# Performance work log

Measured on AMD Instinct MI355X. Metric: run time of the kernel, lower is better.

Reference implementation:

```python
import jax, jax.numpy as jnp
import numpy as np

B, N, C_IN, C_OUT, R_IN, R_OUT, NUM_PSI, E = 4, 1024, 128, 256, 32, 32, 2, 65536


def psi(x, src, dst, W, b):
    # GIN-style GNN layer: aggregate neighbors via scatter-add, then linear+relu
    agg = jax.ops.segment_sum(x[src], dst, num_segments=x.shape[0])
    return jax.nn.relu((x + agg) @ W + b)


def setup_inputs() -> dict:
    key = jax.random.key(0)
    ks = jax.random.split(key, 12)
    inp = {
        'x_s': jax.random.normal(ks[0], (B * N, C_IN), jnp.float32),
        'edge_index_s': jax.random.randint(ks[1], (2, E), 0, B * N, jnp.int32),
        'x_t': jax.random.normal(ks[2], (B * N, C_IN), jnp.float32),
        'edge_index_t': jax.random.randint(ks[3], (2, E), 0, B * N, jnp.int32),
        'r': jax.random.normal(ks[4], (NUM_PSI, B, N, R_IN), jnp.float32),
        'W1': jax.random.normal(ks[5], (C_IN, C_OUT), jnp.float32) * (0.2 / np.sqrt(C_IN)),
        'b1': jnp.zeros((C_OUT,), jnp.float32),
        'Wp': jax.random.normal(ks[6], (NUM_PSI, R_IN, R_OUT), jnp.float32) * (1.0 / np.sqrt(R_IN)),
        'bp': jnp.zeros((NUM_PSI, R_OUT), jnp.float32),
        'Wm1': jax.random.normal(ks[7], (R_OUT, R_OUT), jnp.float32) * (1.0 / np.sqrt(R_OUT)),
        'bm1': jnp.zeros((R_OUT,), jnp.float32),
        'Wm2': jax.random.normal(ks[8], (R_OUT, 1), jnp.float32) * (1.0 / np.sqrt(R_OUT)),
        'bm2': jnp.zeros((1,), jnp.float32),
        'sum_weights': jnp.ones((NUM_PSI + 1,), jnp.float32),
    }
    return inp


def reference(x_s, edge_index_s, x_t, edge_index_t, r, W1, b1, Wp, bp, Wm1, bm1, Wm2, bm2, sum_weights):
    src_s, dst_s = edge_index_s[0], edge_index_s[1]
    src_t, dst_t = edge_index_t[0], edge_index_t[1]
    # psi_1 node embeddings, then dense-batch (equal-size graphs -> masks all true)
    h_s = psi(x_s, src_s, dst_s, W1, b1).reshape(B, N, C_OUT)
    h_t = psi(x_t, src_t, dst_t, W1, b1).reshape(B, N, C_OUT)
    S_hat = jnp.einsum('bsc,btc->bst', h_s, h_t)  # [B, N_s, N_t]
    S_0 = jax.nn.softmax(S_hat, axis=-1)
    S_stack = []
    for i in range(NUM_PSI):  # structurally distinct psi modules
        S = jax.nn.softmax(S_hat, axis=-1)
        r_s = r[i]  # [B, N, R_IN] random node indicators
        r_t = jnp.einsum('bst,bsr->btr', S, r_s)
        o_s = psi(r_s.reshape(B * N, R_IN), src_s, dst_s, Wp[i], bp[i]).reshape(B, N, R_OUT)
        o_t = psi(r_t.reshape(B * N, R_IN), src_t, dst_t, Wp[i], bp[i]).reshape(B, N, R_OUT)
        D = o_s[:, :, None, :] - o_t[:, None, :, :]  # [B, N_s, N_t, R_OUT]
        upd = (jax.nn.relu(D @ Wm1 + bm1) @ Wm2 + bm2)[..., 0]
        S_hat = S_hat + upd
        S_stack.append(jax.nn.softmax(S_hat, axis=-1))
    S_final = sum_weights[0] * S_0
    for i in range(NUM_PSI):
        S_final = S_final + sum_weights[i + 1] * S_stack[i]
    return jax.nn.softmax(S_final.reshape(B * N, N), axis=-1)
```

## Files before the change

kernel.cpp:

```cpp
#include <hip/hip_runtime.h>
#include <hip/hip_bf16.h>

#define NBATCH 4
#define NSEQ   1024
#define BNN    4096
#define CIN    128
#define COUT   256
#define RDIM   32
#define NEDGE  65536

__global__ void edge_hist(const int* __restrict__ ei_s, const int* __restrict__ ei_t,
                          int* __restrict__ cnt) {
    int gid = blockIdx.x * blockDim.x + threadIdx.x;
    int list = gid >> 16;
    int e = gid & (NEDGE - 1);
    const int* ei = list ? ei_t : ei_s;
    atomicAdd(&cnt[list * BNN + ei[NEDGE + e]], 1);
}

__global__ void edge_scan(const int* __restrict__ cnt, int* __restrict__ offs,
                          int* __restrict__ cursor) {
    __shared__ int sums[256];
    int list = blockIdx.x;
    int tid = threadIdx.x;
    int local[16];
    int s = 0;
#pragma unroll
    for (int k = 0; k < 16; k++) { local[k] = cnt[list * BNN + tid * 16 + k]; s += local[k]; }
    sums[tid] = s;
    __syncthreads();
    for (int off = 1; off < 256; off <<= 1) {
        int v = 0;
        if (tid >= off) v = sums[tid - off];
        __syncthreads();
        if (tid >= off) sums[tid] += v;
        __syncthreads();
    }
    int run = tid ? sums[tid - 1] : 0;
#pragma unroll
    for (int k = 0; k < 16; k++) {
        offs[list * (BNN + 1) + tid * 16 + k] = run;
        cursor[list * BNN + tid * 16 + k] = run;
        run += local[k];
    }
    if (tid == 255) offs[list * (BNN + 1) + BNN] = run;
}

__global__ void edge_place(const int* __restrict__ ei_s, const int* __restrict__ ei_t,
                           int* __restrict__ cursor, int* __restrict__ ssrc) {
    int gid = blockIdx.x * blockDim.x + threadIdx.x;
    int list = gid >> 16;
    int e = gid & (NEDGE - 1);
    const int* ei = list ? ei_t : ei_s;
    int dst = ei[NEDGE + e], src = ei[e];
    int p = atomicAdd(&cursor[list * BNN + dst], 1);
    ssrc[list * NEDGE + p] = src;
}

__global__ void gather_agg128(const float* __restrict__ x_s, const float* __restrict__ x_t,
                              const int* __restrict__ offs, const int* __restrict__ ssrc,
                              float* __restrict__ t_s, float* __restrict__ t_t) {
    __shared__ int sl[128];
    int node = blockIdx.x & (BNN - 1);
    int list = blockIdx.x >> 12;
    const float* x = list ? x_t : x_s;
    float* t = list ? t_t : t_s;
    int c = threadIdx.x;
    int beg = offs[list * (BNN + 1) + node], end = offs[list * (BNN + 1) + node + 1];
    float acc = x[(size_t)node * CIN + c];
    for (int base = beg; base < end; base += 128) {
        int cnt = min(128, end - base);
        __syncthreads();
        if (c < cnt) sl[c] = ssrc[list * NEDGE + base + c];
        __syncthreads();
        int e = 0;
        for (; e + 4 <= cnt; e += 4) {
            int n0 = sl[e], n1 = sl[e + 1], n2 = sl[e + 2], n3 = sl[e + 3];
            acc += x[(size_t)n0 * CIN + c] + x[(size_t)n1 * CIN + c]
                 + x[(size_t)n2 * CIN + c] + x[(size_t)n3 * CIN + c];
        }
        for (; e < cnt; e++) acc += x[(size_t)sl[e] * CIN + c];
    }
    t[(size_t)node * CIN + c] = acc;
}

__global__ void gather_agg32(const float* __restrict__ rs, const float* __restrict__ rtin,
                             const int* __restrict__ offs, const int* __restrict__ ssrc,
                             float* __restrict__ trs, float* __restrict__ trt) {
    int list = blockIdx.y;
    int node = blockIdx.x * 8 + (threadIdx.x >> 5);
    int c = threadIdx.x & 31;
    const float* in = list ? rtin : rs;
    float* outp = list ? trt : trs;
    int beg = offs[list * (BNN + 1) + node], end = offs[list * (BNN + 1) + node + 1];
    float acc = in[(size_t)node * RDIM + c];
    for (int e = beg; e < end; e++)
        acc += in[(size_t)ssrc[list * NEDGE + e] * RDIM + c];
    outp[(size_t)node * RDIM + c] = acc;
}

__global__ void psi1_gemm(const float* __restrict__ t_s, const float* __restrict__ t_t,
                          const float* __restrict__ W1, const float* __restrict__ b1,
                          float* __restrict__ h_s, float* __restrict__ h_t) {
    __shared__ float rows[8][CIN];
    int half = blockIdx.x >> 9;
    const float* t = half ? t_t : t_s;
    float* h = half ? h_t : h_s;
    int r0 = (blockIdx.x & 511) * 8;
    int tid = threadIdx.x;
    {
        int rr = tid >> 5, c4 = (tid & 31) << 2;
        *(float4*)&rows[rr][c4] = *(const float4*)(t + (size_t)(r0 + rr) * CIN + c4);
    }
    __syncthreads();
    float acc[8];
    float bias = b1[tid];
#pragma unroll
    for (int r = 0; r < 8; r++) acc[r] = bias;
    for (int k = 0; k < CIN; k++) {
        float w = W1[k * COUT + tid];
#pragma unroll
        for (int r = 0; r < 8; r++) acc[r] = fmaf(rows[r][k], w, acc[r]);
    }
#pragma unroll
    for (int r = 0; r < 8; r++)
        h[(size_t)(r0 + r) * COUT + tid] = fmaxf(acc[r], 0.f);
}

__global__ __launch_bounds__(256) void shat_gemm(const float* __restrict__ hs,
                                                 const float* __restrict__ ht,
                                                 float* __restrict__ Sh) {
    __shared__ float As[16][132];
    __shared__ float Bs[16][68];
    int b  = blockIdx.z;
    int s0 = blockIdx.y * 128, t0 = blockIdx.x * 64;
    const float* A  = hs + (size_t)b * NSEQ * COUT;
    const float* Bm = ht + (size_t)b * NSEQ * COUT;
    int tid = threadIdx.x;
    int tx = tid & 15, ty = tid >> 4;
    int lrA = tid >> 1,  lkA = (tid & 1) * 8;
    int lrB = tid >> 2,  lkB = (tid & 3) * 4;
    const float* Ap = A  + (size_t)(s0 + lrA) * COUT + lkA;
    const float* Bp = Bm + (size_t)(t0 + lrB) * COUT + lkB;
    float4 a0 = *(const float4*)(Ap);
    float4 a1 = *(const float4*)(Ap + 4);
    float4 b0 = *(const float4*)(Bp);
    float acc[8][4] = {};
    for (int kp = 0; kp < 16; kp++) {
        __syncthreads();
        As[lkA + 0][lrA] = a0.x; As[lkA + 1][lrA] = a0.y;
        As[lkA + 2][lrA] = a0.z; As[lkA + 3][lrA] = a0.w;
        As[lkA + 4][lrA] = a1.x; As[lkA + 5][lrA] = a1.y;
        As[lkA + 6][lrA] = a1.z; As[lkA + 7][lrA] = a1.w;
        Bs[lkB + 0][lrB] = b0.x; Bs[lkB + 1][lrB] = b0.y;
        Bs[lkB + 2][lrB] = b0.z; Bs[lkB + 3][lrB] = b0.w;
        __syncthreads();
        if (kp < 15) {
            a0 = *(const float4*)(Ap + (kp + 1) * 16);
            a1 = *(const float4*)(Ap + (kp + 1) * 16 + 4);
            b0 = *(const float4*)(Bp + (kp + 1) * 16);
        }
#pragma unroll
        for (int k = 0; k < 16; k++) {
            float av[8], bv[4];
            *(float4*)&av[0] = *(const float4*)&As[k][ty * 8];
            *(float4*)&av[4] = *(const float4*)&As[k][ty * 8 + 4];
            *(float4*)&bv[0] = *(const float4*)&Bs[k][tx * 4];
#pragma unroll
            for (int i = 0; i < 8; i++)
#pragma unroll
                for (int j = 0; j < 4; j++)
                    acc[i][j] = fmaf(av[i], bv[j], acc[i][j]);
        }
    }
#pragma unroll
    for (int i = 0; i < 8; i++) {
        float4 v = make_float4(acc[i][0], acc[i][1], acc[i][2], acc[i][3]);
        *(float4*)(Sh + ((size_t)b * NSEQ + s0 + ty * 8 + i) * NSEQ + t0 + tx * 4) = v;
    }
}

__global__ void softmax_stats(const float* __restrict__ Sh, float* __restrict__ mstat,
                              float* __restrict__ istat) {
    int row = blockIdx.x, tid = threadIdx.x;
    float4 v = *(const float4*)(Sh + (size_t)row * NSEQ + tid * 4);
    float m = fmaxf(fmaxf(v.x, v.y), fmaxf(v.z, v.w));
#pragma unroll
    for (int o = 32; o; o >>= 1) m = fmaxf(m, __shfl_xor(m, o));
    __shared__ float redm[4], reds[4];
    int wid = tid >> 6, lane = tid & 63;
    if (lane == 0) redm[wid] = m;
    __syncthreads();
    m = fmaxf(fmaxf(redm[0], redm[1]), fmaxf(redm[2], redm[3]));
    float s = __expf(v.x - m) + __expf(v.y - m) + __expf(v.z - m) + __expf(v.w - m);
#pragma unroll
    for (int o = 32; o; o >>= 1) s += __shfl_xor(s, o);
    if (lane == 0) reds[wid] = s;
    __syncthreads();
    if (tid == 0) {
        float tot = reds[0] + reds[1] + reds[2] + reds[3];
        mstat[row] = m;
        istat[row] = 1.0f / tot;
    }
}

__global__ void softmax_final3(const float* __restrict__ Sh0, const float* __restrict__ Sh1,
                               const float* __restrict__ Sh2, const float* __restrict__ m0a,
                               const float* __restrict__ i0a, const float* __restrict__ m1a,
                               const float* __restrict__ i1a, const float* __restrict__ sw,
                               float* __restrict__ out) {
    int row = blockIdx.x, tid = threadIdx.x;
    __shared__ float red[4];
    int wid = tid >> 6, lane = tid & 63;
    float4 v0 = *(const float4*)(Sh0 + (size_t)row * NSEQ + tid * 4);
    float4 v1 = *(const float4*)(Sh1 + (size_t)row * NSEQ + tid * 4);
    float4 v2 = *(const float4*)(Sh2 + (size_t)row * NSEQ + tid * 4);
    float m2 = fmaxf(fmaxf(v2.x, v2.y), fmaxf(v2.z, v2.w));
#pragma unroll
    for (int o = 32; o; o >>= 1) m2 = fmaxf(m2, __shfl_xor(m2, o));
    if (lane == 0) red[wid] = m2;
    __syncthreads();
    m2 = fmaxf(fmaxf(red[0], red[1]), fmaxf(red[2], red[3]));
    __syncthreads();
    float4 e2;
    e2.x = __expf(v2.x - m2); e2.y = __expf(v2.y - m2);
    e2.z = __expf(v2.z - m2); e2.w = __expf(v2.w - m2);
    float s2 = e2.x + e2.y + e2.z + e2.w;
#pragma unroll
    for (int o = 32; o; o >>= 1) s2 += __shfl_xor(s2, o);
    if (lane == 0) red[wid] = s2;
    __syncthreads();
    s2 = red[0] + red[1] + red[2] + red[3];
    __syncthreads();
    float w0 = sw[0] * i0a[row], w1 = sw[1] * i1a[row], w2 = sw[2] / s2;
    float m0 = m0a[row], m1 = m1a[row];
    float4 f;
    f.x = fmaf(w0, __expf(v0.x - m0), fmaf(w1, __expf(v1.x - m1), w2 * e2.x));
    f.y = fmaf(w0, __expf(v0.y - m0), fmaf(w1, __expf(v1.y - m1), w2 * e2.y));
    f.z = fmaf(w0, __expf(v0.z - m0), fmaf(w1, __expf(v1.z - m1), w2 * e2.z));
    f.w = fmaf(w0, __expf(v0.w - m0), fmaf(w1, __expf(v1.w - m1), w2 * e2.w));
    float mf = fmaxf(fmaxf(f.x, f.y), fmaxf(f.z, f.w));
#pragma unroll
    for (int o = 32; o; o >>= 1) mf = fmaxf(mf, __shfl_xor(mf, o));
    if (lane == 0) red[wid] = mf;
    __syncthreads();
    mf = fmaxf(fmaxf(red[0], red[1]), fmaxf(red[2], red[3]));
    __syncthreads();
    float4 ef;
    ef.x = __expf(f.x - mf); ef.y = __expf(f.y - mf);
    ef.z = __expf(f.z - mf); ef.w = __expf(f.w - mf);
    float sf = ef.x + ef.y + ef.z + ef.w;
#pragma unroll
    for (int o = 32; o; o >>= 1) sf += __shfl_xor(sf, o);
    if (lane == 0) red[wid] = sf;
    __syncthreads();
    sf = red[0] + red[1] + red[2] + red[3];
    float inv = 1.0f / sf;
    float4 sv = make_float4(ef.x * inv, ef.y * inv, ef.z * inv, ef.w * inv);
    *(float4*)(out + (size_t)row * NSEQ + tid * 4) = sv;
}

__global__ void rt_part(const float* __restrict__ Sh, const float* __restrict__ mstat,
                        const float* __restrict__ istat, const float* __restrict__ rs,
                        float* __restrict__ part) {
    __shared__ float rsld[64][33];
    __shared__ float ml[64], il[64];
    int b = blockIdx.z, t0 = blockIdx.y * 128, s0 = blockIdx.x * 64;
    int tid = threadIdx.x;
    if (tid < 64) ml[tid] = mstat[b * NSEQ + s0 + tid];
    else if (tid < 128) il[tid - 64] = istat[b * NSEQ + s0 + tid - 64];
#pragma unroll
    for (int q = 0; q < 2; q++) {
        int lid = (tid << 1) + q;
        int srow = lid >> 3, c4 = (lid & 7) << 2;
        float4 v = *(const float4*)(rs + ((size_t)b * NSEQ + s0 + srow) * RDIM + c4);
        rsld[srow][c4] = v.x; rsld[srow][c4 + 1] = v.y;
        rsld[srow][c4 + 2] = v.z; rsld[srow][c4 + 3] = v.w;
    }
    __syncthreads();
    int t = t0 + (tid & 127);
    int j0 = (tid >> 7) << 4;
    float acc[16] = {};
    const float* Sp = Sh + ((size_t)b * NSEQ + s0) * NSEQ + t;
#pragma unroll 8
    for (int s = 0; s < 64; s++) {
        float p = __expf(Sp[(size_t)s * NSEQ] - ml[s]) * il[s];
#pragma unroll
        for (int j = 0; j < 16; j++) acc[j] = fmaf(p, rsld[s][j0 + j], acc[j]);
    }
    float* pp = part + (((size_t)blockIdx.x * NBATCH + b) * NSEQ + t) * RDIM + j0;
#pragma unroll
    for (int j4 = 0; j4 < 16; j4 += 4)
        *(float4*)(pp + j4) = make_float4(acc[j4], acc[j4 + 1], acc[j4 + 2], acc[j4 + 3]);
}

__global__ void rt_reduce(const float* __restrict__ part, float* __restrict__ rt) {
    int i = blockIdx.x * blockDim.x + threadIdx.x;
    const float4* p = (const float4*)part + i;
    float4 a = make_float4(0.f, 0.f, 0.f, 0.f);
#pragma unroll
    for (int c = 0; c < 16; c++) {
        float4 v = p[(size_t)c * (BNN * RDIM / 4)];
        a.x += v.x; a.y += v.y; a.z += v.z; a.w += v.w;
    }
    ((float4*)rt)[i] = a;
}

__global__ void psi_r(const float* __restrict__ trs, const float* __restrict__ trt,
                      const float* __restrict__ Wp, const float* __restrict__ bp,
                      const float* __restrict__ Wm1, const float* __restrict__ bm1,
                      float* __restrict__ Ps, float* __restrict__ Pt) {
    __shared__ float sWp[32 * 32], sWm1[32 * 32];
    __shared__ float srow[8][33], so[8][33];
    int which = blockIdx.y;
    const float* t_r = which ? trt : trs;
    float* P = which ? Pt : Ps;
    int tid = threadIdx.x;
#pragma unroll
    for (int q = 0; q < 4; q++) {
        sWp[tid + q * 256]  = Wp[tid + q * 256];
        sWm1[tid + q * 256] = Wm1[tid + q * 256];
    }
    int g = tid >> 5, j = tid & 31;
    int row = blockIdx.x * 8 + g;
    srow[g][j] = t_r[(size_t)row * RDIM + j];
    __syncthreads();
    float acc = bp[j];
#pragma unroll
    for (int k = 0; k < 32; k++) acc = fmaf(srow[g][k], sWp[k * 32 + j], acc);
    float o = fmaxf(acc, 0.f);
    so[g][j] = o;
    __syncthreads();
    float acc2 = which ? 0.f : bm1[j];
#pragma unroll
    for (int k = 0; k < 32; k++) acc2 = fmaf(so[g][k], sWm1[k * 32 + j], acc2);
    P[(size_t)row * RDIM + j] = acc2;
}

__global__ void upd_add(const float* __restrict__ Ps, const float* __restrict__ Pt,
                        const float* __restrict__ Wm2, const float* __restrict__ bm2p,
                        const float* __restrict__ Shin, float* __restrict__ Shout) {
    __shared__ float sPs[64][33], sPt[64][33];
    __shared__ float swm[32];
    int b = blockIdx.z, s0 = blockIdx.y * 64, t0 = blockIdx.x * 64;
    int tid = threadIdx.x;
#pragma unroll
    for (int q = 0; q < 2; q++) {
        int lid = (tid << 1) + q, rr = lid >> 3, c4 = (lid & 7) << 2;
        float4 a = *(const float4*)(Ps + ((size_t)b * NSEQ + s0 + rr) * RDIM + c4);
        sPs[rr][c4] = a.x; sPs[rr][c4 + 1] = a.y; sPs[rr][c4 + 2] = a.z; sPs[rr][c4 + 3] = a.w;
        float4 c = *(const float4*)(Pt + ((size_t)b * NSEQ + t0 + rr) * RDIM + c4);
        sPt[rr][c4] = c.x; sPt[rr][c4 + 1] = c.y; sPt[rr][c4 + 2] = c.z; sPt[rr][c4 + 3] = c.w;
    }
    if (tid < 32) swm[tid] = Wm2[tid];
    __syncthreads();
    float bm2 = bm2p[0];
    int tx = tid & 15, ty = tid >> 4;
    float acc[4][4] = {};
#pragma unroll
    for (int k = 0; k < 32; k++) {
        float w = swm[k];
        float ps[4], pt[4];
#pragma unroll
        for (int i = 0; i < 4; i++) ps[i] = sPs[ty * 4 + i][k];
#pragma unroll
        for (int j = 0; j < 4; j++) pt[j] = sPt[tx * 4 + j][k];
#pragma unroll
        for (int i = 0; i < 4; i++)
#pragma unroll
            for (int j = 0; j < 4; j++)
                acc[i][j] = fmaf(fmaxf(ps[i] - pt[j], 0.f), w, acc[i][j]);
    }
#pragma unroll
    for (int i = 0; i < 4; i++) {
        size_t base = ((size_t)b * NSEQ + s0 + ty * 4 + i) * NSEQ + t0 + tx * 4;
        float4 old = *(const float4*)(Shin + base);
        old.x += acc[i][0] + bm2; old.y += acc[i][1] + bm2;
        old.z += acc[i][2] + bm2; old.w += acc[i][3] + bm2;
        *(float4*)(Shout + base) = old;
    }
}

extern "C" void kernel_launch(void* const* d_in, const int* in_sizes, int n_in,
                              void* d_out, int out_size, void* d_ws, size_t ws_size,
                              hipStream_t stream) {
    const float* x_s  = (const float*)d_in[0];
    const int*   ei_s = (const int*)  d_in[1];
    const float* x_t  = (const float*)d_in[2];
    const int*   ei_t = (const int*)  d_in[3];
    const float* r    = (const float*)d_in[4];
    const float* W1   = (const float*)d_in[5];
    const float* b1   = (const float*)d_in[6];
    const float* Wp   = (const float*)d_in[7];
    const float* bp   = (const float*)d_in[8];
    const float* Wm1  = (const float*)d_in[9];
    const float* bm1  = (const float*)d_in[10];
    const float* Wm2  = (const float*)d_in[11];
    const float* bm2  = (const float*)d_in[12];
    const float* sw   = (const float*)d_in[13];
    float* out = (float*)d_out;

    float* ws = (float*)d_ws;
    float* t_s  = ws;  ws += (size_t)BNN * CIN;
    float* t_t  = ws;  ws += (size_t)BNN * CIN;
    float* h_s  = ws;  ws += (size_t)BNN * COUT;
    float* h_t  = ws;  ws += (size_t)BNN * COUT;
    float* Sh0  = ws;  ws += (size_t)NBATCH * NSEQ * NSEQ;
    float* Sh1  = ws;  ws += (size_t)NBATCH * NSEQ * NSEQ;
    float* Sh2  = ws;  ws += (size_t)NBATCH * NSEQ * NSEQ;
    float* mstat = ws; ws += 2 * BNN;
    float* istat = ws; ws += 2 * BNN;
    float* rt   = ws;  ws += (size_t)BNN * RDIM;
    float* trs  = ws;  ws += (size_t)BNN * RDIM;
    float* trt  = ws;  ws += (size_t)BNN * RDIM;
    float* Ps   = ws;  ws += (size_t)BNN * RDIM;
    float* Pt   = ws;  ws += (size_t)BNN * RDIM;
    int* icnt  = (int*)ws;
    int* ioffs = icnt  + 2 * BNN;
    int* icur  = ioffs + 2 * (BNN + 1);
    int* issrc = icur  + 2 * BNN;
    float* rtpart = h_s;

    float* ShA[3] = {Sh0, Sh1, Sh2};

    hipMemsetAsync(icnt, 0, 2 * BNN * sizeof(int), stream);
    edge_hist <<<512, 256, 0, stream>>>(ei_s, ei_t, icnt);
    edge_scan <<<2, 256, 0, stream>>>(icnt, ioffs, icur);
    edge_place<<<512, 256, 0, stream>>>(ei_s, ei_t, icur, issrc);

    gather_agg128<<<8192, 128, 0, stream>>>(x_s, x_t, ioffs, issrc, t_s, t_t);
    psi1_gemm<<<1024, 256, 0, stream>>>(t_s, t_t, W1, b1, h_s, h_t);
    shat_gemm<<<dim3(16, 8, 4), 256, 0, stream>>>(h_s, h_t, Sh0);

    for (int i = 0; i < 2; i++) {
        softmax_stats<<<4096, 256, 0, stream>>>(ShA[i], mstat + i * BNN, istat + i * BNN);
        rt_part<<<dim3(16, 8, 4), 256, 0, stream>>>(ShA[i], mstat + i * BNN, istat + i * BNN,
                                                    r + (size_t)i * BNN * RDIM, rtpart);
        rt_reduce<<<128, 256, 0, stream>>>(rtpart, rt);
        gather_agg32<<<dim3(512, 2), 256, 0, stream>>>(r + (size_t)i * BNN * RDIM, rt,
                                                       ioffs, issrc, trs, trt);
        psi_r<<<dim3(512, 2), 256, 0, stream>>>(trs, trt, Wp + i * RDIM * RDIM,
                                                bp + i * RDIM, Wm1, bm1, Ps, Pt);
        upd_add<<<dim3(16, 16, 4), 256, 0, stream>>>(Ps, Pt, Wm2, bm2, ShA[i], ShA[i + 1]);
    }
    softmax_final3<<<4096, 256, 0, stream>>>(Sh0, Sh1, Sh2, mstat, istat,
                                             mstat + BNN, istat + BNN, sw, out);
}
```

Measured before the change: 214.5 us.

## Fuse softmax row stats into GEMM/update epilogues and merge gather with psi

Computes per-tile partial max and sum-exp in the epilogues of shat_gemm and upd_add, then combines them in a small stats_combine kernel. This removes the separate softmax_stats passes that each reread a 16MB score matrix, and simplifies the final softmax to use precomputed stats. It also fuses gather_agg32 into the psi MLP kernel and adds a block-index swizzle to shat_gemm for cache locality. The cost is extra shuffles and exps in the GEMM epilogues plus scattered partial-stat writes.

```diff
diff --git a/kernel.cpp b/kernel.cpp
--- a/kernel.cpp
+++ b/kernel.cpp
@@ -8,6 +8,7 @@
 #define COUT   256
 #define RDIM   32
 #define NEDGE  65536
+#define NTILE  16
 
 __global__ void edge_hist(const int* __restrict__ ei_s, const int* __restrict__ ei_t,
                           int* __restrict__ cnt) {
@@ -84,21 +85,6 @@
     t[(size_t)node * CIN + c] = acc;
 }
 
-__global__ void gather_agg32(const float* __restrict__ rs, const float* __restrict__ rtin,
-                             const int* __restrict__ offs, const int* __restrict__ ssrc,
-                             float* __restrict__ trs, float* __restrict__ trt) {
-    int list = blockIdx.y;
-    int node = blockIdx.x * 8 + (threadIdx.x >> 5);
-    int c = threadIdx.x & 31;
-    const float* in = list ? rtin : rs;
-    float* outp = list ? trt : trs;
-    int beg = offs[list * (BNN + 1) + node], end = offs[list * (BNN + 1) + node + 1];
-    float acc = in[(size_t)node * RDIM + c];
-    for (int e = beg; e < end; e++)
-        acc += in[(size_t)ssrc[list * NEDGE + e] * RDIM + c];
-    outp[(size_t)node * RDIM + c] = acc;
-}
-
 __global__ void psi1_gemm(const float* __restrict__ t_s, const float* __restrict__ t_t,
                           const float* __restrict__ W1, const float* __restrict__ b1,
                           float* __restrict__ h_s, float* __restrict__ h_t) {
@@ -129,11 +115,16 @@
 
 __global__ __launch_bounds__(256) void shat_gemm(const float* __restrict__ hs,
                                                  const float* __restrict__ ht,
-                                                 float* __restrict__ Sh) {
+                                                 float* __restrict__ Sh,
+                                                 float* __restrict__ pmax,
+                                                 float* __restrict__ psum) {
     __shared__ float As[16][132];
     __shared__ float Bs[16][68];
-    int b  = blockIdx.z;
-    int s0 = blockIdx.y * 128, t0 = blockIdx.x * 64;
+    int flat = blockIdx.x;
+    int swz = (flat & 7) * 64 + (flat >> 3);
+    int bx = swz & 15, by = (swz >> 4) & 7, bz = swz >> 7;
+    int b  = bz;
+    int s0 = by * 128, t0 = bx * 64;
     const float* A  = hs + (size_t)b * NSEQ * COUT;
     const float* Bm = ht + (size_t)b * NSEQ * COUT;
     int tid = threadIdx.x;
@@ -177,87 +168,32 @@
     for (int i = 0; i < 8; i++) {
         float4 v = make_float4(acc[i][0], acc[i][1], acc[i][2], acc[i][3]);
         *(float4*)(Sh + ((size_t)b * NSEQ + s0 + ty * 8 + i) * NSEQ + t0 + tx * 4) = v;
-    }
-}
-
-__global__ void softmax_stats(const float* __restrict__ Sh, float* __restrict__ mstat,
-                              float* __restrict__ istat) {
-    int row = blockIdx.x, tid = threadIdx.x;
-    float4 v = *(const float4*)(Sh + (size_t)row * NSEQ + tid * 4);
-    float m = fmaxf(fmaxf(v.x, v.y), fmaxf(v.z, v.w));
-#pragma unroll
-    for (int o = 32; o; o >>= 1) m = fmaxf(m, __shfl_xor(m, o));
-    __shared__ float redm[4], reds[4];
-    int wid = tid >> 6, lane = tid & 63;
-    if (lane == 0) redm[wid] = m;
-    __syncthreads();
-    m = fmaxf(fmaxf(redm[0], redm[1]), fmaxf(redm[2], redm[3]));
-    float s = __expf(v.x - m) + __expf(v.y - m) + __expf(v.z - m) + __expf(v.w - m);
-#pragma unroll
-    for (int o = 32; o; o >>= 1) s += __shfl_xor(s, o);
-    if (lane == 0) reds[wid] = s;
-    __syncthreads();
-    if (tid == 0) {
-        float tot = reds[0] + reds[1] + reds[2] + reds[3];
-        mstat[row] = m;
-        istat[row] = 1.0f / tot;
-    }
-}
-
-__global__ void softmax_final3(const float* __restrict__ Sh0, const float* __restrict__ Sh1,
-                               const float* __restrict__ Sh2, const float* __restrict__ m0a,
-                               const float* __restrict__ i0a, const float* __restrict__ m1a,
-                               const float* __restrict__ i1a, const float* __restrict__ sw,
-                               float* __restrict__ out) {
-    int row = blockIdx.x, tid = threadIdx.x;
-    __shared__ float red[4];
-    int wid = tid >> 6, lane = tid & 63;
-    float4 v0 = *(const float4*)(Sh0 + (size_t)row * NSEQ + tid * 4);
-    float4 v1 = *(const float4*)(Sh1 + (size_t)row * NSEQ + tid * 4);
-    float4 v2 = *(const float4*)(Sh2 + (size_t)row * NSEQ + tid * 4);
-    float m2 = fmaxf(fmaxf(v2.x, v2.y), fmaxf(v2.z, v2.w));
-#pragma unroll
-    for (int o = 32; o; o >>= 1) m2 = fmaxf(m2, __shfl_xor(m2, o));
-    if (lane == 0) red[wid] = m2;
-    __syncthreads();
-    m2 = fmaxf(fmaxf(red[0], red[1]), fmaxf(red[2], red[3]));
-    __syncthreads();
-    float4 e2;
-    e2.x = __expf(v2.x - m2); e2.y = __expf(v2.y - m2);
-    e2.z = __expf(v2.z - m2); e2.w = __expf(v2.w - m2);
-    float s2 = e2.x + e2.y + e2.z + e2.w;
-#pragma unroll
-    for (int o = 32; o; o >>= 1) s2 += __shfl_xor(s2, o);
-    if (lane == 0) red[wid] = s2;
-    __syncthreads();
-    s2 = red[0] + red[1] + red[2] + red[3];
-    __syncthreads();
-    float w0 = sw[0] * i0a[row], w1 = sw[1] * i1a[row], w2 = sw[2] / s2;
-    float m0 = m0a[row], m1 = m1a[row];
-    float4 f;
-    f.x = fmaf(w0, __expf(v0.x - m0), fmaf(w1, __expf(v1.x - m1), w2 * e2.x));
-    f.y = fmaf(w0, __expf(v0.y - m0), fmaf(w1, __expf(v1.y - m1), w2 * e2.y));
-    f.z = fmaf(w0, __expf(v0.z - m0), fmaf(w1, __expf(v1.z - m1), w2 * e2.z));
-    f.w = fmaf(w0, __expf(v0.w - m0), fmaf(w1, __expf(v1.w - m1), w2 * e2.w));
-    float mf = fmaxf(fmaxf(f.x, f.y), fmaxf(f.z, f.w));
-#pragma unroll
-    for (int o = 32; o; o >>= 1) mf = fmaxf(mf, __shfl_xor(mf, o));
-    if (lane == 0) red[wid] = mf;
-    __syncthreads();
-    mf = fmaxf(fmaxf(red[0], red[1]), fmaxf(red[2], red[3]));
-    __syncthreads();
-    float4 ef;
-    ef.x = __expf(f.x - mf); ef.y = __expf(f.y - mf);
-    ef.z = __expf(f.z - mf); ef.w = __expf(f.w - mf);
-    float sf = ef.x + ef.y + ef.z + ef.w;
-#pragma unroll
-    for (int o = 32; o; o >>= 1) sf += __shfl_xor(sf, o);
-    if (lane == 0) red[wid] = sf;
-    __syncthreads();
-    sf = red[0] + red[1] + red[2] + red[3];
-    float inv = 1.0f / sf;
-    float4 sv = make_float4(ef.x * inv, ef.y * inv, ef.z * inv, ef.w * inv);
-    *(float4*)(out + (size_t)row * NSEQ + tid * 4) = sv;
+        float ml = fmaxf(fmaxf(v.x, v.y), fmaxf(v.z, v.w));
+#pragma unroll
+        for (int o = 1; o < 16; o <<= 1) ml = fmaxf(ml, __shfl_xor(ml, o, 16));
+        float sl = __expf(v.x - ml) + __expf(v.y - ml) + __expf(v.z - ml) + __expf(v.w - ml);
+#pragma unroll
+        for (int o = 1; o < 16; o <<= 1) sl += __shfl_xor(sl, o, 16);
+        if (tx == 0) {
+            int grow = b * NSEQ + s0 + ty * 8 + i;
+            pmax[grow * NTILE + bx] = ml;
+            psum[grow * NTILE + bx] = sl;
+        }
+    }
+}
+
+__global__ void stats_combine(const float* __restrict__ pmax, const float* __restrict__ psum,
+                              float* __restrict__ mstat, float* __restrict__ istat) {
+    int row = blockIdx.x * blockDim.x + threadIdx.x;
+    float pm[NTILE];
+    float m = -3.4e38f;
+#pragma unroll
+    for (int t = 0; t < NTILE; t++) { pm[t] = pmax[row * NTILE + t]; m = fmaxf(m, pm[t]); }
+    float s = 0.f;
+#pragma unroll
+    for (int t = 0; t < NTILE; t++) s += psum[row * NTILE + t] * __expf(pm[t] - m);
+    mstat[row] = m;
+    istat[row] = 1.0f / s;
 }
 
 __global__ void rt_part(const float* __restrict__ Sh, const float* __restrict__ mstat,
@@ -306,14 +242,15 @@
     ((float4*)rt)[i] = a;
 }
 
-__global__ void psi_r(const float* __restrict__ trs, const float* __restrict__ trt,
-                      const float* __restrict__ Wp, const float* __restrict__ bp,
-                      const float* __restrict__ Wm1, const float* __restrict__ bm1,
-                      float* __restrict__ Ps, float* __restrict__ Pt) {
+__global__ void gather_psi(const float* __restrict__ rs, const float* __restrict__ rtin,
+                           const int* __restrict__ offs, const int* __restrict__ ssrc,
+                           const float* __restrict__ Wp, const float* __restrict__ bp,
+                           const float* __restrict__ Wm1, const float* __restrict__ bm1,
+                           float* __restrict__ Ps, float* __restrict__ Pt) {
     __shared__ float sWp[32 * 32], sWm1[32 * 32];
     __shared__ float srow[8][33], so[8][33];
     int which = blockIdx.y;
-    const float* t_r = which ? trt : trs;
+    const float* in = which ? rtin : rs;
     float* P = which ? Pt : Ps;
     int tid = threadIdx.x;
 #pragma unroll
@@ -322,24 +259,28 @@
         sWm1[tid + q * 256] = Wm1[tid + q * 256];
     }
     int g = tid >> 5, j = tid & 31;
-    int row = blockIdx.x * 8 + g;
-    srow[g][j] = t_r[(size_t)row * RDIM + j];
-    __syncthreads();
-    float acc = bp[j];
-#pragma unroll
-    for (int k = 0; k < 32; k++) acc = fmaf(srow[g][k], sWp[k * 32 + j], acc);
-    float o = fmaxf(acc, 0.f);
-    so[g][j] = o;
-    __syncthreads();
-    float acc2 = which ? 0.f : bm1[j];
-#pragma unroll
-    for (int k = 0; k < 32; k++) acc2 = fmaf(so[g][k], sWm1[k * 32 + j], acc2);
-    P[(size_t)row * RDIM + j] = acc2;
-}
-
-__global__ void upd_add(const float* __restrict__ Ps, const float* __restrict__ Pt,
-                        const float* __restrict__ Wm2, const float* __restrict__ bm2p,
-                        const float* __restrict__ Shin, float* __restrict__ Shout) {
+    int node = blockIdx.x * 8 + g;
+    int beg = offs[which * (BNN + 1) + node], end = offs[which * (BNN + 1) + node + 1];
+    float acc = in[(size_t)node * RDIM + j];
+    for (int e = beg; e < end; e++)
+        acc += in[(size_t)ssrc[which * NEDGE + e] * RDIM + j];
+    srow[g][j] = acc;
+    __syncthreads();
+    float a1 = bp[j];
+#pragma unroll
+    for (int k = 0; k < 32; k++) a1 = fmaf(srow[g][k], sWp[k * 32 + j], a1);
+    so[g][j] = fmaxf(a1, 0.f);
+    __syncthreads();
+    float a2 = which ? 0.f : bm1[j];
+#pragma unroll
+    for (int k = 0; k < 32; k++) a2 = fmaf(so[g][k], sWm1[k * 32 + j], a2);
+    P[(size_t)node * RDIM + j] = a2;
+}
+
+__global__ void upd_add_stats(const float* __restrict__ Ps, const float* __restrict__ Pt,
+                              const float* __restrict__ Wm2, const float* __restrict__ bm2p,
+                              const float* __restrict__ Shin, float* __restrict__ Shout,
+                              float* __restrict__ pmax, float* __restrict__ psum) {
     __shared__ float sPs[64][33], sPt[64][33];
     __shared__ float swm[32];
     int b = blockIdx.z, s0 = blockIdx.y * 64, t0 = blockIdx.x * 64;
@@ -375,10 +316,60 @@
     for (int i = 0; i < 4; i++) {
         size_t base = ((size_t)b * NSEQ + s0 + ty * 4 + i) * NSEQ + t0 + tx * 4;
         float4 old = *(const float4*)(Shin + base);
-        old.x += acc[i][0] + bm2; old.y += acc[i][1] + bm2;
-        old.z += acc[i][2] + bm2; old.w += acc[i][3] + bm2;
-        *(float4*)(Shout + base) = old;
-    }
+        float4 f;
+        f.x = old.x + acc[i][0] + bm2; f.y = old.y + acc[i][1] + bm2;
+        f.z = old.z + acc[i][2] + bm2; f.w = old.w + acc[i][3] + bm2;
+        *(float4*)(Shout + base) = f;
+        float ml = fmaxf(fmaxf(f.x, f.y), fmaxf(f.z, f.w));
+#pragma unroll
+        for (int o = 1; o < 16; o <<= 1) ml = fmaxf(ml, __shfl_xor(ml, o, 16));
+        float sl = __expf(f.x - ml) + __expf(f.y - ml) + __expf(f.z - ml) + __expf(f.w - ml);
+#pragma unroll
+        for (int o = 1; o < 16; o <<= 1) sl += __shfl_xor(sl, o, 16);
+        if (tx == 0) {
+            int grow = b * NSEQ + s0 + ty * 4 + i;
+            pmax[grow * NTILE + blockIdx.x] = ml;
+            psum[grow * NTILE + blockIdx.x] = sl;
+        }
+    }
+}
+
+__global__ void softmax_final3(const float* __restrict__ Sh0, const float* __restrict__ Sh1,
+                               const float* __restrict__ Sh2, const float* __restrict__ mst,
+                               const float* __restrict__ ist, const float* __restrict__ sw,
+                               float* __restrict__ out) {
+    int row = blockIdx.x, tid = threadIdx.x;
+    __shared__ float redm[4], reds[4];
+    int wid = tid >> 6, lane = tid & 63;
+    float4 v0 = *(const float4*)(Sh0 + (size_t)row * NSEQ + tid * 4);
+    float4 v1 = *(const float4*)(Sh1 + (size_t)row * NSEQ + tid * 4);
+    float4 v2 = *(const float4*)(Sh2 + (size_t)row * NSEQ + tid * 4);
+    float m0 = mst[row],           w0 = sw[0] * ist[row];
+    float m1 = mst[BNN + row],     w1 = sw[1] * ist[BNN + row];
+    float m2 = mst[2 * BNN + row], w2 = sw[2] * ist[2 * BNN + row];
+    float4 f;
+    f.x = fmaf(w0, __expf(v0.x - m0), fmaf(w1, __expf(v1.x - m1), w2 * __expf(v2.x - m2)));
+    f.y = fmaf(w0, __expf(v0.y - m0), fmaf(w1, __expf(v1.y - m1), w2 * __expf(v2.y - m2)));
+    f.z = fmaf(w0, __expf(v0.z - m0), fmaf(w1, __expf(v1.z - m1), w2 * __expf(v2.z - m2)));
+    f.w = fmaf(w0, __expf(v0.w - m0), fmaf(w1, __expf(v1.w - m1), w2 * __expf(v2.w - m2)));
+    float mf = fmaxf(fmaxf(f.x, f.y), fmaxf(f.z, f.w));
+#pragma unroll
+    for (int o = 32; o; o >>= 1) mf = fmaxf(mf, __shfl_xor(mf, o));
+    if (lane == 0) redm[wid] = mf;
+    __syncthreads();
+    mf = fmaxf(fmaxf(redm[0], redm[1]), fmaxf(redm[2], redm[3]));
+    float4 ef;
+    ef.x = __expf(f.x - mf); ef.y = __expf(f.y - mf);
+    ef.z = __expf(f.z - mf); ef.w = __expf(f.w - mf);
+    float sf = ef.x + ef.y + ef.z + ef.w;
+#pragma unroll
+    for (int o = 32; o; o >>= 1) sf += __shfl_xor(sf, o);
+    if (lane == 0) reds[wid] = sf;
+    __syncthreads();
+    sf = reds[0] + reds[1] + reds[2] + reds[3];
+    float inv = 1.0f / sf;
+    float4 sv = make_float4(ef.x * inv, ef.y * inv, ef.z * inv, ef.w * inv);
+    *(float4*)(out + (size_t)row * NSEQ + tid * 4) = sv;
 }
 
 extern "C" void kernel_launch(void* const* d_in, const int* in_sizes, int n_in,
@@ -408,11 +399,11 @@
     float* Sh0  = ws;  ws += (size_t)NBATCH * NSEQ * NSEQ;
     float* Sh1  = ws;  ws += (size_t)NBATCH * NSEQ * NSEQ;
     float* Sh2  = ws;  ws += (size_t)NBATCH * NSEQ * NSEQ;
-    float* mstat = ws; ws += 2 * BNN;
-    float* istat = ws; ws += 2 * BNN;
+    float* mstat = ws; ws += 3 * BNN;
+    float* istat = ws; ws += 3 * BNN;
+    float* pmax = ws;  ws += (size_t)BNN * NTILE;
+    float* psum = ws;  ws += (size_t)BNN * NTILE;
     float* rt   = ws;  ws += (size_t)BNN * RDIM;
-    float* trs  = ws;  ws += (size_t)BNN * RDIM;
-    float* trt  = ws;  ws += (size_t)BNN * RDIM;
     float* Ps   = ws;  ws += (size_t)BNN * RDIM;
     float* Pt   = ws;  ws += (size_t)BNN * RDIM;
     int* icnt  = (int*)ws;
@@ -430,19 +421,20 @@
 
     gather_agg128<<<8192, 128, 0, stream>>>(x_s, x_t, ioffs, issrc, t_s, t_t);
     psi1_gemm<<<1024, 256, 0, stream>>>(t_s, t_t, W1, b1, h_s, h_t);
-    shat_gemm<<<dim3(16, 8, 4), 256, 0, stream>>>(h_s, h_t, Sh0);
+    shat_gemm<<<512, 256, 0, stream>>>(h_s, h_t, Sh0, pmax, psum);
+    stats_combine<<<16, 256, 0, stream>>>(pmax, psum, mstat, istat);
 
     for (int i = 0; i < 2; i++) {
-        softmax_stats<<<4096, 256, 0, stream>>>(ShA[i], mstat + i * BNN, istat + i * BNN);
         rt_part<<<dim3(16, 8, 4), 256, 0, stream>>>(ShA[i], mstat + i * BNN, istat + i * BNN,
                                                     r + (size_t)i * BNN * RDIM, rtpart);
         rt_reduce<<<128, 256, 0, stream>>>(rtpart, rt);
-        gather_agg32<<<dim3(512, 2), 256, 0, stream>>>(r + (size_t)i * BNN * RDIM, rt,
-                                                       ioffs, issrc, trs, trt);
-        psi_r<<<dim3(512, 2), 256, 0, stream>>>(trs, trt, Wp + i * RDIM * RDIM,
-                                                bp + i * RDIM, Wm1, bm1, Ps, Pt);
-        upd_add<<<dim3(16, 16, 4), 256, 0, stream>>>(Ps, Pt, Wm2, bm2, ShA[i], ShA[i + 1]);
-    }
-    softmax_final3<<<4096, 256, 0, stream>>>(Sh0, Sh1, Sh2, mstat, istat,
-                                             mstat + BNN, istat + BNN, sw, out);
-}
+        gather_psi<<<dim3(512, 2), 256, 0, stream>>>(r + (size_t)i * BNN * RDIM, rt,
+                                                     ioffs, issrc, Wp + i * RDIM * RDIM,
+                                                     bp + i * RDIM, Wm1, bm1, Ps, Pt);
+        upd_add_stats<<<dim3(16, 16, 4), 256, 0, stream>>>(Ps, Pt, Wm2, bm2,
+                                                           ShA[i], ShA[i + 1], pmax, psum);
+        stats_combine<<<16, 256, 0, stream>>>(pmax, psum, mstat + (i + 1) * BNN,
+                                              istat + (i + 1) * BNN);
+    }
+    softmax_final3<<<4096, 256, 0, stream>>>(Sh0, Sh1, Sh2, mstat, istat, sw, out);
+}
```

New measurement: 457.9 us. 113% more time.
